# Optimization experiments

Measured on AMD Instinct MI355X. Metric: run time of the kernel, lower is better.

Reference implementation:

```python
import jax, jax.numpy as jnp
import numpy as np

SIZE = 5      # LCN local region (ZF2013)
K_STAB = 1.0  # stability constant added to variance
STRIDE = 2
PAD = 3       # (stride-1 + kernel_size-1)//2 with kernel_size=7, stride=2
RADIUS = 0.1  # filter RMS renormalization radius


def _renorm(w):
    # renormalize filters whose RMS exceeds RADIUS back to RADIUS (no_grad in torch)
    rms = jnp.sqrt(jnp.mean(w * w, axis=(1, 2, 3)))
    scale = jnp.where(rms > RADIUS, RADIUS / rms, 1.0)
    return w * jax.lax.stop_gradient(scale)[:, None, None, None]


def _box(x):
    # depthwise 5x5 box filter (mean over local window), zero padding like F.conv2d
    C = x.shape[1]
    k = jnp.ones((C, 1, SIZE, SIZE), x.dtype) / (SIZE * SIZE)
    return jax.lax.conv_general_dilated(
        x, k, (1, 1), [(SIZE // 2, SIZE // 2)] * 2,
        feature_group_count=C,
        dimension_numbers=('NCHW', 'OIHW', 'NCHW'))


def _forward_core(x, weight, bias):
    w = _renorm(weight)
    y = jax.lax.conv_general_dilated(
        x, w, (STRIDE, STRIDE), [(PAD, PAD)] * 2,
        dimension_numbers=('NCHW', 'OIHW', 'NCHW')) + bias[None, :, None, None]
    # local contrast normalization (vectorized over channels; torch loops per-channel)
    mean = _box(y)
    centered = y - mean
    var = _box(centered * centered)
    y = centered / jnp.sqrt(var + K_STAB)
    return jax.nn.relu(y)


def _maxpool2(x):
    # 2x2 maxpool with torch-style flat (H*W) indices per channel plane
    B, C, H, W = x.shape
    xw = x.reshape(B, C, H // 2, 2, W // 2, 2).transpose(0, 1, 2, 4, 3, 5)
    xw = xw.reshape(B, C, H // 2, W // 2, 4)
    out = jnp.max(xw, axis=-1)
    loc = jnp.argmax(xw, axis=-1)
    hp = jnp.arange(H // 2)[:, None]
    wp = jnp.arange(W // 2)[None, :]
    idx = (2 * hp + loc // 2) * W + (2 * wp + loc % 2)
    return out, idx.astype(jnp.int32)


def setup_inputs() -> dict:
    key = jax.random.key(0)
    k1, k2, k3 = jax.random.split(key, 3)
    x = jax.random.normal(k1, (16, 3, 224, 224), jnp.float32)
    weight = jax.random.normal(k2, (96, 3, 7, 7), jnp.float32) * 0.1
    bias = jax.random.normal(k3, (96,), jnp.float32) * 0.01
    return {"x": x, "weight": weight, "bias": bias}


def reference(x, weight, bias):
    pre_pool = _forward_core(x, weight, bias)  # [16,96,112,112]
    out, indices = _maxpool2(pre_pool)          # [16,96,56,56]
    return out, pre_pool, indices
```

## Files before the change

### kernel.cpp

```cpp
#include <hip/hip_runtime.h>

#define OC    96
#define IH    224
#define IW    224
#define OHH   112
#define OWW   112
#define NIMG  16

typedef __attribute__((ext_vector_type(8))) short bf16x8;
typedef __attribute__((ext_vector_type(4))) float f32x4;

static __device__ inline unsigned short f2bf(float f) {
    unsigned int u = __float_as_uint(f);
    unsigned int rounded = u + 0x7fff + ((u >> 16) & 1);
    return (unsigned short)(rounded >> 16);
}

__global__ __launch_bounds__(64) void wfrag_kernel(const float* __restrict__ w,
                                                   uint4* __restrict__ wfrag) {
    const int bid = blockIdx.x;
    const int mt = bid / 6, ch = bid - mt * 6;
    const int lane = threadIdx.x;
    const int oc = mt * 16 + (lane & 15);
    const int u  = lane >> 4;

    float ssq = 0.f;
    for (int k = 0; k < 147; ++k) {
        float v = w[oc * 147 + k];
        ssq += v * v;
    }
    float rms   = sqrtf(ssq * (1.0f / 147.0f));
    float scale = (rms > 0.1f) ? (0.1f / rms) : 1.0f;

    const int U = ch * 4 + u;
    unsigned short h[8];
    #pragma unroll
    for (int j = 0; j < 8; ++j) {
        float val = 0.f;
        if (U < 21 && j < 7) {
            int c  = U / 7;
            int kh = U - 7 * c;
            val = w[oc * 147 + c * 49 + kh * 7 + j] * scale;
        }
        h[j] = f2bf(val);
    }
    uint4 o;
    o.x = (unsigned)h[0] | ((unsigned)h[1] << 16);
    o.y = (unsigned)h[2] | ((unsigned)h[3] << 16);
    o.z = (unsigned)h[4] | ((unsigned)h[5] << 16);
    o.w = (unsigned)h[6] | ((unsigned)h[7] << 16);
    wfrag[(mt * 6 + ch) * 64 + lane] = o;
}

__global__ __launch_bounds__(512, 2) void conv_mfma_kernel(const float* __restrict__ x,
                                                           const uint4* __restrict__ wfrag,
                                                           const float* __restrict__ bias,
                                                           unsigned short* __restrict__ ypb) {
    __shared__ float patch[3 * 21 * 40];

    const int tid  = threadIdx.x;
    const int bx   = blockIdx.x;
    const int img  = blockIdx.y;
    const int tx = bx % 7, ty = bx / 7;
    const int ow0 = 16 * tx, oh0 = 8 * ty;
    const int ih0 = 2 * oh0 - 3, iwb = 2 * ow0 - 3;
    const float* xim = x + (size_t)img * 3 * IH * IW;

    for (int i = tid; i < 3 * 21 * 40; i += 512) {
        int c   = i / 840;
        int rem = i - c * 840;
        int r   = rem / 40;
        int cc  = rem - r * 40;
        int ih = ih0 + r, iw = iwb + cc;
        float v = 0.f;
        if ((unsigned)ih < IH && (unsigned)iw < IW) v = xim[(c * IH + ih) * IW + iw];
        patch[i] = v;
    }

    const int wv   = tid >> 6;
    const int lane = tid & 63;
    const int wm = wv >> 2;
    const int wn = wv & 3;
    const int n  = lane & 15;
    const int u  = lane >> 4;

    f32x4 acc[3][2];
    #pragma unroll
    for (int a = 0; a < 3; ++a)
        #pragma unroll
        for (int t = 0; t < 2; ++t) acc[a][t] = (f32x4){0.f, 0.f, 0.f, 0.f};

    uint4 anxt[3];
    #pragma unroll
    for (int a = 0; a < 3; ++a)
        anxt[a] = wfrag[(((wm * 3 + a) * 6) + 0) * 64 + lane];

    __syncthreads();

    #pragma unroll
    for (int ch = 0; ch < 6; ++ch) {
        uint4 acur[3] = {anxt[0], anxt[1], anxt[2]};
        if (ch < 5) {
            #pragma unroll
            for (int a = 0; a < 3; ++a)
                anxt[a] = wfrag[(((wm * 3 + a) * 6) + ch + 1) * 64 + lane];
        }
        int U = ch * 4 + u;
        int cq = 0, khq = 0;
        if (U < 21) { cq = U / 7; khq = U - 7 * cq; }
        #pragma unroll
        for (int nt = 0; nt < 2; ++nt) {
            const int t = 2 * wn + nt;
            const float* bp = &patch[cq * 840 + (2 * t + khq) * 40 + 2 * n];
            float2 p0 = *(const float2*)(bp + 0);
            float2 p1 = *(const float2*)(bp + 2);
            float2 p2 = *(const float2*)(bp + 4);
            float2 p3 = *(const float2*)(bp + 6);
            bf16x8 bfr;
            bfr[0] = (short)f2bf(p0.x); bfr[1] = (short)f2bf(p0.y);
            bfr[2] = (short)f2bf(p1.x); bfr[3] = (short)f2bf(p1.y);
            bfr[4] = (short)f2bf(p2.x); bfr[5] = (short)f2bf(p2.y);
            bfr[6] = (short)f2bf(p3.x); bfr[7] = (short)f2bf(p3.y);
            #pragma unroll
            for (int a = 0; a < 3; ++a) {
                bf16x8 afr = *(bf16x8*)&acur[a];
                acc[a][nt] = __builtin_amdgcn_mfma_f32_16x16x32_bf16(afr, bfr, acc[a][nt], 0, 0, 0);
            }
        }
    }

    #pragma unroll
    for (int a = 0; a < 3; ++a) {
        const int mt = wm * 3 + a;
        const int ocb = mt * 16 + u * 4;
        float4 bi = *(const float4*)(bias + ocb);
        float bv[4] = {bi.x, bi.y, bi.z, bi.w};
        #pragma unroll
        for (int nt = 0; nt < 2; ++nt) {
            const int oh = oh0 + 2 * wn + nt;
            unsigned short* yb = ypb + (((size_t)img * OC + ocb) * OHH + oh) * OWW + ow0 + n;
            #pragma unroll
            for (int r = 0; r < 4; ++r)
                yb[(size_t)r * (OHH * OWW)] = f2bf(acc[a][nt][r] + bv[r]);
        }
    }
}

__global__ __launch_bounds__(256) void lcn_pool_kernel(const unsigned short* __restrict__ y,
                                                       float* __restrict__ outp,
                                                       float* __restrict__ prep,
                                                       float* __restrict__ idxp) {
    const int tid   = threadIdx.x;
    const int band  = tid >> 6;
    const int lane  = tid & 63;
    const int plane = blockIdx.x;
    const int r0    = band * 28;
    const int c0    = lane * 2;
    const bool colv = (lane < 56);

    const unsigned short* yp = y + (size_t)plane * (OHH * OWW);
    float* pp  = prep + (size_t)plane * (OHH * OWW);
    float* op_ = outp + (size_t)plane * (56 * 56);
    float* ip_ = idxp + (size_t)plane * (56 * 56);

    const int lm = (lane + 63) & 63;
    const int lp = (lane + 1) & 63;

    float2 hs0{0,0}, hs1{0,0}, hs2{0,0}, hs3{0,0}, hs4{0,0};
    float2 q0{0,0},  q1{0,0},  q2{0,0},  q3{0,0},  q4{0,0};
    float2 y0{0,0},  y1{0,0},  y2{0,0};
    float2 ct0{0,0}, ct1{0,0}, ct2{0,0};
    float2 prev{0,0};

    #pragma unroll 1
    for (int i = 0; i < 36; ++i) {
        const int irow = r0 - 4 + i;
        float2 v = {0.f, 0.f};
        if ((unsigned)irow < OHH && colv) {
            unsigned int pr = *(const unsigned int*)(yp + irow * OWW + c0);
            v.x = __uint_as_float(pr << 16);
            v.y = __uint_as_float(pr & 0xffff0000u);
        }

        float Lx = __shfl(v.x, lm, 64), Ly = __shfl(v.y, lm, 64);
        float Rx = __shfl(v.x, lp, 64), Ry = __shfl(v.y, lp, 64);
        float2 hs_new;
        hs_new.x = Lx + Ly + v.x + v.y + Rx;
        hs_new.y = Ly + v.x + v.y + Rx + Ry;
        hs0 = hs1; hs1 = hs2; hs2 = hs3; hs3 = hs4; hs4 = hs_new;
        y0 = y1; y1 = y2; y2 = v;

        if (i >= 4) {
            const int m = irow - 2;
            float2 mean;
            mean.x = (hs0.x + hs1.x + hs2.x + hs3.x + hs4.x) * 0.04f;
            mean.y = (hs0.y + hs1.y + hs2.y + hs3.y + hs4.y) * 0.04f;
            float2 ct;
            ct.x = y0.x - mean.x;
            ct.y = y0.y - mean.y;
            if ((unsigned)m >= OHH || !colv) { ct.x = 0.f; ct.y = 0.f; }

            float cLx = __shfl(ct.x, lm, 64), cLy = __shfl(ct.y, lm, 64);
            float cRx = __shfl(ct.x, lp, 64), cRy = __shfl(ct.y, lp, 64);
            float2 q_new;
            q_new.x = cLx*cLx + cLy*cLy + ct.x*ct.x + ct.y*ct.y + cRx*cRx;
            q_new.y = cLy*cLy + ct.x*ct.x + ct.y*ct.y + cRx*cRx + cRy*cRy;
            q0 = q1; q1 = q2; q2 = q3; q3 = q4; q4 = q_new;
            ct0 = ct1; ct1 = ct2; ct2 = ct;

            if (i >= 8) {
                const int o = irow - 4;
                float2 var;
                var.x = (q0.x + q1.x + q2.x + q3.x + q4.x) * 0.04f;
                var.y = (q0.y + q1.y + q2.y + q3.y + q4.y) * 0.04f;
                float vx = fmaxf(ct0.x * rsqrtf(var.x + 1.0f), 0.f);
                float vy = fmaxf(ct0.y * rsqrtf(var.y + 1.0f), 0.f);
                if (colv) {
                    float2 pv = {vx, vy};
                    *(float2*)(pp + o * OWW + c0) = pv;
                }
                if (o & 1) {
                    float best = prev.x; int loc = 0;
                    if (prev.y > best) { best = prev.y; loc = 1; }
                    if (vx     > best) { best = vx;     loc = 2; }
                    if (vy     > best) { best = vy;     loc = 3; }
                    int idx = (o - 1 + (loc >> 1)) * OWW + (c0 + (loc & 1));
                    if (colv) {
                        size_t oo = (size_t)(o >> 1) * 56 + lane;
                        op_[oo] = best;
                        ip_[oo] = (float)idx;
                    }
                }
                prev.x = vx; prev.y = vy;
            }
        }
    }
}

extern "C" void kernel_launch(void* const* d_in, const int* in_sizes, int n_in,
                              void* d_out, int out_size, void* d_ws, size_t ws_size,
                              hipStream_t stream) {
    const float* x    = (const float*)d_in[0];
    const float* w    = (const float*)d_in[1];
    const float* bias = (const float*)d_in[2];

    unsigned short* y = (unsigned short*)d_ws;
    uint4* wfrag = (uint4*)((char*)d_ws + (size_t)NIMG * OC * OHH * OWW * 2);

    float* outp = (float*)d_out;
    float* prep = outp + (size_t)NIMG * OC * 56 * 56;
    float* idxp = prep + (size_t)NIMG * OC * OHH * OWW;

    wfrag_kernel<<<dim3(36), dim3(64), 0, stream>>>(w, wfrag);
    conv_mfma_kernel<<<dim3(98, NIMG), dim3(512), 0, stream>>>(x, wfrag, bias, y);
    lcn_pool_kernel<<<dim3(NIMG * OC), dim3(256), 0, stream>>>(y, outp, prep, idxp);
}
```

Baseline: 78.63 us.

## Swap MFMA operand roles so each wave covers one output row and all channels

The conv MFMA kernel now gives each of the 8 waves one output row and all 96 output channels (6 accumulator tiles), instead of a 2x4 split over channel groups and row pairs. Each wave builds a single input fragment per k-chunk and reuses it across 6 weight fragments, which cuts LDS reads and bf16 conversions per MFMA. The activation is now operand A and the weights operand B, so each lane holds 4 consecutive output columns and writes them as one 8-byte store instead of scattered 2-byte stores. The cost is more weight-fragment registers per wave and a switch to the library bf16 conversion, which may round differently from the hand-written routine.

```diff
diff --git a/kernel.cpp b/kernel.cpp
--- a/kernel.cpp
+++ b/kernel.cpp
@@ -1,4 +1,5 @@
 #include <hip/hip_runtime.h>
+#include <hip/hip_bf16.h>
 
 #define OC    96
 #define IH    224
@@ -19,9 +20,9 @@
 __global__ __launch_bounds__(64) void wfrag_kernel(const float* __restrict__ w,
                                                    uint4* __restrict__ wfrag) {
     const int bid = blockIdx.x;
-    const int mt = bid / 6, ch = bid - mt * 6;
+    const int oct = bid / 6, ch = bid - oct * 6;
     const int lane = threadIdx.x;
-    const int oc = mt * 16 + (lane & 15);
+    const int oc = oct * 16 + (lane & 15);
     const int u  = lane >> 4;
 
     float ssq = 0.f;
@@ -49,7 +50,7 @@
     o.y = (unsigned)h[2] | ((unsigned)h[3] << 16);
     o.z = (unsigned)h[4] | ((unsigned)h[5] << 16);
     o.w = (unsigned)h[6] | ((unsigned)h[7] << 16);
-    wfrag[(mt * 6 + ch) * 64 + lane] = o;
+    wfrag[(oct * 6 + ch) * 64 + lane] = o;
 }
 
 __global__ __launch_bounds__(512, 2) void conv_mfma_kernel(const float* __restrict__ x,
@@ -77,72 +78,72 @@
         patch[i] = v;
     }
 
-    const int wv   = tid >> 6;
+    const int t    = tid >> 6;
     const int lane = tid & 63;
-    const int wm = wv >> 2;
-    const int wn = wv & 3;
-    const int n  = lane & 15;
-    const int u  = lane >> 4;
-
-    f32x4 acc[3][2];
-    #pragma unroll
-    for (int a = 0; a < 3; ++a)
-        #pragma unroll
-        for (int t = 0; t < 2; ++t) acc[a][t] = (f32x4){0.f, 0.f, 0.f, 0.f};
-
-    uint4 anxt[3];
-    #pragma unroll
-    for (int a = 0; a < 3; ++a)
-        anxt[a] = wfrag[(((wm * 3 + a) * 6) + 0) * 64 + lane];
+    const int m    = lane & 15;
+    const int u    = lane >> 4;
+
+    int rb[6];
+    #pragma unroll
+    for (int ch = 0; ch < 6; ++ch) {
+        int U  = 4 * ch + u;
+        int cq = (U >= 7) + (U >= 14);
+        int khq = U - 7 * cq;
+        rb[ch] = (U < 21) ? (cq * 840 + khq * 40) : 0;
+    }
+
+    f32x4 acc[6];
+    #pragma unroll
+    for (int a = 0; a < 6; ++a) acc[a] = (f32x4){0.f, 0.f, 0.f, 0.f};
+
+    uint4 wnxt[6];
+    #pragma unroll
+    for (int a = 0; a < 6; ++a) wnxt[a] = wfrag[(a * 6 + 0) * 64 + lane];
 
     __syncthreads();
 
     #pragma unroll
     for (int ch = 0; ch < 6; ++ch) {
-        uint4 acur[3] = {anxt[0], anxt[1], anxt[2]};
+        uint4 wcur[6] = {wnxt[0], wnxt[1], wnxt[2], wnxt[3], wnxt[4], wnxt[5]};
         if (ch < 5) {
             #pragma unroll
-            for (int a = 0; a < 3; ++a)
-                anxt[a] = wfrag[(((wm * 3 + a) * 6) + ch + 1) * 64 + lane];
-        }
-        int U = ch * 4 + u;
-        int cq = 0, khq = 0;
-        if (U < 21) { cq = U / 7; khq = U - 7 * cq; }
+            for (int a = 0; a < 6; ++a) wnxt[a] = wfrag[(a * 6 + ch + 1) * 64 + lane];
+        }
+        const float* bp = &patch[rb[ch] + t * 80 + 2 * m];
+        float2 p0 = *(const float2*)(bp + 0);
+        float2 p1 = *(const float2*)(bp + 2);
+        float2 p2 = *(const float2*)(bp + 4);
+        float2 p3 = *(const float2*)(bp + 6);
+        __hip_bfloat16 c0 = (__hip_bfloat16)p0.x, c1 = (__hip_bfloat16)p0.y;
+        __hip_bfloat16 c2 = (__hip_bfloat16)p1.x, c3 = (__hip_bfloat16)p1.y;
+        __hip_bfloat16 c4 = (__hip_bfloat16)p2.x, c5 = (__hip_bfloat16)p2.y;
+        __hip_bfloat16 c6 = (__hip_bfloat16)p3.x, c7 = (__hip_bfloat16)p3.y;
+        bf16x8 xfr;
+        xfr[0] = __hip_bfloat16_raw(c0).x; xfr[1] = __hip_bfloat16_raw(c1).x;
+        xfr[2] = __hip_bfloat16_raw(c2).x; xfr[3] = __hip_bfloat16_raw(c3).x;
+        xfr[4] = __hip_bfloat16_raw(c4).x; xfr[5] = __hip_bfloat16_raw(c5).x;
+        xfr[6] = __hip_bfloat16_raw(c6).x; xfr[7] = __hip_bfloat16_raw(c7).x;
         #pragma unroll
-        for (int nt = 0; nt < 2; ++nt) {
-            const int t = 2 * wn + nt;
-            const float* bp = &patch[cq * 840 + (2 * t + khq) * 40 + 2 * n];
-            float2 p0 = *(const float2*)(bp + 0);
-            float2 p1 = *(const float2*)(bp + 2);
-            float2 p2 = *(const float2*)(bp + 4);
-            float2 p3 = *(const float2*)(bp + 6);
-            bf16x8 bfr;
-            bfr[0] = (short)f2bf(p0.x); bfr[1] = (short)f2bf(p0.y);
-            bfr[2] = (short)f2bf(p1.x); bfr[3] = (short)f2bf(p1.y);
-            bfr[4] = (short)f2bf(p2.x); bfr[5] = (short)f2bf(p2.y);
-            bfr[6] = (short)f2bf(p3.x); bfr[7] = (short)f2bf(p3.y);
-            #pragma unroll
-            for (int a = 0; a < 3; ++a) {
-                bf16x8 afr = *(bf16x8*)&acur[a];
-                acc[a][nt] = __builtin_amdgcn_mfma_f32_16x16x32_bf16(afr, bfr, acc[a][nt], 0, 0, 0);
-            }
-        }
-    }
-
-    #pragma unroll
-    for (int a = 0; a < 3; ++a) {
-        const int mt = wm * 3 + a;
-        const int ocb = mt * 16 + u * 4;
-        float4 bi = *(const float4*)(bias + ocb);
-        float bv[4] = {bi.x, bi.y, bi.z, bi.w};
-        #pragma unroll
-        for (int nt = 0; nt < 2; ++nt) {
-            const int oh = oh0 + 2 * wn + nt;
-            unsigned short* yb = ypb + (((size_t)img * OC + ocb) * OHH + oh) * OWW + ow0 + n;
-            #pragma unroll
-            for (int r = 0; r < 4; ++r)
-                yb[(size_t)r * (OHH * OWW)] = f2bf(acc[a][nt][r] + bv[r]);
-        }
+        for (int a = 0; a < 6; ++a) {
+            bf16x8 wfr = *(bf16x8*)&wcur[a];
+            acc[a] = __builtin_amdgcn_mfma_f32_16x16x32_bf16(xfr, wfr, acc[a], 0, 0, 0);
+        }
+    }
+
+    const int oh = oh0 + t;
+    const int ow = ow0 + u * 4;
+    #pragma unroll
+    for (int a = 0; a < 6; ++a) {
+        const int oc = a * 16 + m;
+        const float bv = bias[oc];
+        unsigned short h0 = f2bf(acc[a][0] + bv);
+        unsigned short h1 = f2bf(acc[a][1] + bv);
+        unsigned short h2 = f2bf(acc[a][2] + bv);
+        unsigned short h3 = f2bf(acc[a][3] + bv);
+        uint2 st;
+        st.x = (unsigned)h0 | ((unsigned)h1 << 16);
+        st.y = (unsigned)h2 | ((unsigned)h3 << 16);
+        *(uint2*)(ypb + (((size_t)img * OC + oc) * OHH + oh) * OWW + ow) = st;
     }
 }
 
@@ -191,14 +192,14 @@
         y0 = y1; y1 = y2; y2 = v;
 
         if (i >= 4) {
-            const int m = irow - 2;
+            const int mrow = irow - 2;
             float2 mean;
             mean.x = (hs0.x + hs1.x + hs2.x + hs3.x + hs4.x) * 0.04f;
             mean.y = (hs0.y + hs1.y + hs2.y + hs3.y + hs4.y) * 0.04f;
             float2 ct;
             ct.x = y0.x - mean.x;
             ct.y = y0.y - mean.y;
-            if ((unsigned)m >= OHH || !colv) { ct.x = 0.f; ct.y = 0.f; }
+            if ((unsigned)mrow >= OHH || !colv) { ct.x = 0.f; ct.y = 0.f; }
 
             float cLx = __shfl(ct.x, lm, 64), cLy = __shfl(ct.y, lm, 64);
             float cRx = __shfl(ct.x, lp, 64), cRy = __shfl(ct.y, lp, 64);
```

After: 90.07 us. 1.15x slower.
